# Kernel optimization log

Measured on AMD Instinct MI355X. Metric: run time of the kernel, lower is better.

## Reference

```python
import jax, jax.numpy as jnp
import numpy as np

B, S, D, H, L = 64, 512, 512, 512, 2  # batch, seq_len, input_size, hidden_size, num_layers


def setup_inputs() -> dict:
    key = jax.random.key(0)
    ks = jax.random.split(key, 4)
    s = 0.03  # keep gate pre-activations in the non-saturated range
    x = jax.random.normal(ks[0], (B, S, D), jnp.float32)
    h = jnp.zeros((B, L, H), jnp.float32)
    Wr = jax.random.normal(ks[1], (L, D + H, H), jnp.float32) * s
    Wz = jax.random.normal(ks[2], (L, D + H, H), jnp.float32) * s
    Wh = jax.random.normal(ks[3], (L, D + H, H), jnp.float32) * s
    br = jnp.zeros((L, H), jnp.float32)
    bz = jnp.zeros((L, H), jnp.float32)
    bh = jnp.zeros((L, H), jnp.float32)
    return dict(x=x, h=h, Wr=Wr, br=br, Wz=Wz, bz=bz, Wh=Wh, bh=bh)


def _gru_layer(x, h0, Wr, br, Wz, bz, Wh, bh):
    # Linear(cat(x, h)) == x @ W[:Din] + h @ W[Din:] + b ; precompute the x part
    Din = x.shape[-1]
    gx_r = jnp.einsum('bsd,dh->bsh', x, Wr[:Din]) + br  # [B,S,H]
    gx_z = jnp.einsum('bsd,dh->bsh', x, Wz[:Din]) + bz
    gx_h = jnp.einsum('bsd,dh->bsh', x, Wh[:Din]) + bh
    Wrh, Wzh, Whh = Wr[Din:], Wz[Din:], Wh[Din:]  # [H,H]

    def step(h, gates):
        gr, gz, gh = gates  # each [B,H]
        r = jax.nn.sigmoid(gr + h @ Wrh)
        z = jax.nn.sigmoid(gz + h @ Wzh)
        h_tilde = jnp.tanh(gh + (r * h) @ Whh)
        h = (1.0 - z) * h + z * h_tilde
        return h, h

    hT, ys = jax.lax.scan(
        step, h0,
        (gx_r.swapaxes(0, 1), gx_z.swapaxes(0, 1), gx_h.swapaxes(0, 1)))
    return ys.swapaxes(0, 1), hT  # [B,S,H], [B,H]


def reference(x, h, Wr, br, Wz, bz, Wh, bh):
    inp = x
    finals = []
    for l in range(L):
        inp, hT = _gru_layer(inp, h[:, l], Wr[l], br[l], Wz[l], bz[l], Wh[l], bh[l])
        finals.append(hT)
    return inp, jnp.stack(finals, axis=1)  # y:[B,S,H], final_h:[B,L,H]
```

## Files before the change

kernel.cpp:

```cpp
#include <hip/hip_runtime.h>

typedef unsigned int uint;
typedef unsigned short u16;
typedef short s16x8 __attribute__((ext_vector_type(8)));
typedef float f32x4 __attribute__((ext_vector_type(4)));
typedef uint u32x4 __attribute__((ext_vector_type(4)));

#define MFMA16(a, b, c) __builtin_amdgcn_mfma_f32_16x16x32_bf16((a), (b), (c), 0, 0, 0)

static const size_t OFF_SYNC = 0;
static const size_t OFF_HB   = 2048;
static const size_t OFF_RHB  = 526336;
static const size_t OFF_WT   = 1050624;
static const size_t OFF_YS0  = 7342080;
static const size_t OFF_GX   = 40896512;
static const size_t GX_ELEMS = (size_t)512 * 64 * 1536;

__device__ __forceinline__ short f2bf(float x) {
  uint u = __builtin_bit_cast(uint, x);
  u = u + 0x7fffu + ((u >> 16) & 1u);
  return (short)(u >> 16);
}
__device__ __forceinline__ float bf2f(u16 v) {
  uint u = ((uint)v) << 16;
  return __builtin_bit_cast(float, u);
}

__device__ __forceinline__ u32x4 ld16(const void* p) {
  u32x4 r;
  asm volatile("global_load_dwordx4 %0, %1, off" : "=v"(r) : "v"(p));
  return r;
}
__device__ __forceinline__ uint ld4u(const void* p) {
  uint r;
  asm volatile("global_load_dword %0, %1, off" : "=v"(r) : "v"(p));
  return r;
}
__device__ __forceinline__ uint ld2x(const void* p) {
  uint r;
  asm volatile("global_load_ushort %0, %1, off" : "=v"(r) : "v"(p));
  return r;
}
__device__ __forceinline__ void st4(void* p, uint v) {
  asm volatile("global_store_dword %0, %1, off" :: "v"(p), "v"(v));
}
__device__ __forceinline__ void st2(void* p, u16 v) {
  uint x = v;
  asm volatile("global_store_short %0, %1, off" :: "v"(p), "v"(x));
}
__device__ __forceinline__ u32x4 ld16c(const void* p) {
  u32x4 r;
  asm volatile("global_load_dwordx4 %0, %1, off sc0 sc1" : "=v"(r) : "v"(p));
  return r;
}
__device__ __forceinline__ void st2c(void* p, u16 v) {
  uint x = v;
  asm volatile("global_store_short %0, %1, off sc0 sc1" :: "v"(p), "v"(x));
}
__device__ __forceinline__ void waitv0() {
  asm volatile("s_waitcnt vmcnt(0)" ::: "memory");
  __builtin_amdgcn_sched_barrier(0);
}

template <int GXBF>
__device__ __forceinline__ float upk(uint v) {
  if constexpr (GXBF) return bf2f((u16)v);
  else return __builtin_bit_cast(float, v);
}

__global__ void sentinel_kernel(float* __restrict__ out, float v) {
  out[threadIdx.x] = v;
}

__global__ void init_kernel(const float* __restrict__ h_in, u16* __restrict__ hb,
                            int* __restrict__ sync) {
  int idx = blockIdx.x * 256 + threadIdx.x;
  if (idx < 512) sync[idx] = 0;
  for (int i = idx; i < 2 * 64 * 512; i += gridDim.x * 256) {
    int l = i >> 15, b = (i >> 9) & 63, c = i & 511;
    int q = b >> 4, ob = b & 15;
    hb[((l * 4 + q) * 4 + 0) * 8192 + ob * 512 + c] = (u16)f2bf(h_in[(b * 2 + l) * 512 + c]);
  }
}

__global__ void convert_w_kernel(const float* __restrict__ Wr, const float* __restrict__ Wz,
                                 const float* __restrict__ Wh, u16* __restrict__ WT) {
  int idx = blockIdx.x * 256 + threadIdx.x;
  int n = idx & 511, k = (idx >> 9) & 1023, lg = idx >> 19;
  int l = (lg >= 3) ? 1 : 0, g = lg - l * 3;
  const float* W = (g == 0 ? Wr : (g == 1 ? Wz : Wh)) + (size_t)l * 1024 * 512;
  WT[((size_t)lg * 512 + n) * 1024 + k] = (u16)f2bf(W[k * 512 + n]);
}

template <int GXBF>
__global__ __launch_bounds__(256) void proj_kernel(
    const float* __restrict__ A, const u16* __restrict__ WT,
    const float* __restrict__ br, const float* __restrict__ bz, const float* __restrict__ bh,
    void* __restrict__ gx) {
  __shared__ u16 Alds[128 * 64];
  __shared__ u16 Blds[128 * 64];
  const int tid = threadIdx.x;
  const int wave = tid >> 6, lane = tid & 63;
  const int lan15 = lane & 15, lanhi = lane >> 4;
  const int mb = blockIdx.x & 255, nb = blockIdx.x >> 8;
  const int m0 = mb * 128, n0 = nb * 128;
  const int wm = (wave >> 1) * 64, wn = (wave & 1) * 64;

  const f32x4 z4 = {0.f, 0.f, 0.f, 0.f};
  f32x4 acc[4][4];
#pragma unroll
  for (int i = 0; i < 4; ++i)
#pragma unroll
    for (int j = 0; j < 4; ++j) acc[i][j] = z4;

  for (int kb = 0; kb < 512; kb += 64) {
    __syncthreads();
#pragma unroll
    for (int p = 0; p < 4; ++p) {
      int idx = p * 256 + tid;
      int row = idx >> 3, slot = idx & 7;
      const float* src = A + (size_t)(m0 + row) * 512 + kb + slot * 8;
      float4 v0 = *(const float4*)src;
      float4 v1 = *(const float4*)(src + 4);
      u16 tmp[8] = {(u16)f2bf(v0.x), (u16)f2bf(v0.y), (u16)f2bf(v0.z), (u16)f2bf(v0.w),
                    (u16)f2bf(v1.x), (u16)f2bf(v1.y), (u16)f2bf(v1.z), (u16)f2bf(v1.w)};
      *(uint4*)((char*)Alds + row * 128 + ((slot ^ (row & 7)) * 16)) = *(uint4*)tmp;
    }
#pragma unroll
    for (int p = 0; p < 4; ++p) {
      int idx = p * 256 + tid;
      int row = idx >> 3, slot = idx & 7;
      int ng = n0 + row, g = ng >> 9, nc = ng & 511;
      uint4 v = *(const uint4*)(WT + ((size_t)g * 512 + nc) * 1024 + kb + slot * 8);
      *(uint4*)((char*)Blds + row * 128 + ((slot ^ (row & 7)) * 16)) = v;
    }
    __syncthreads();
#pragma unroll
    for (int ks = 0; ks < 2; ++ks) {
      s16x8 af[4], bfr[4];
#pragma unroll
      for (int f = 0; f < 4; ++f) {
        int rowA = wm + f * 16 + lan15;
        af[f] = *(const s16x8*)((const char*)Alds + rowA * 128 + (((ks * 4 + lanhi) ^ (rowA & 7)) * 16));
        int rowB = wn + f * 16 + lan15;
        bfr[f] = *(const s16x8*)((const char*)Blds + rowB * 128 + (((ks * 4 + lanhi) ^ (rowB & 7)) * 16));
      }
#pragma unroll
      for (int mf = 0; mf < 4; ++mf)
#pragma unroll
        for (int nf = 0; nf < 4; ++nf)
          acc[mf][nf] = MFMA16(af[mf], bfr[nf], acc[mf][nf]);
    }
  }
#pragma unroll
  for (int nf = 0; nf < 4; ++nf) {
    int n = n0 + wn + nf * 16 + lan15;
    int g = n >> 9, nc = n & 511;
    float bias = (g == 0 ? br[nc] : (g == 1 ? bz[nc] : bh[nc]));
#pragma unroll
    for (int mf = 0; mf < 4; ++mf) {
#pragma unroll
      for (int q = 0; q < 4; ++q) {
        int m = m0 + wm + mf * 16 + lanhi * 4 + q;
        int s = m & 511, b = m >> 9;
        size_t e = (size_t)(s * 64 + b) * 1536 + n;
        float v = acc[mf][nf][q] + bias;
        if constexpr (GXBF) ((u16*)gx)[e] = (u16)f2bf(v);
        else ((float*)gx)[e] = v;
      }
    }
  }
}

__device__ __forceinline__ void gbarA(int* bar, int target) {
  asm volatile("s_waitcnt vmcnt(0)" ::: "memory");
  __syncthreads();
  if (threadIdx.x == 0) {
    int one = 1;
    asm volatile("global_atomic_add %0, %1, off" :: "v"(bar), "v"(one) : "memory");
    int v, zero = 0, iter = 0;
    do {
      __builtin_amdgcn_s_sleep(1);
      asm volatile("global_atomic_add %0, %1, %2, off sc0\n\ts_waitcnt vmcnt(0)"
                   : "=v"(v) : "v"(bar), "v"(zero) : "memory");
    } while (v < target && ++iter < (1 << 17));
  }
  __syncthreads();
  __builtin_amdgcn_sched_barrier(0);
}
__device__ __forceinline__ void bar_arrive(int* bar) {
  asm volatile("s_waitcnt vmcnt(0)" ::: "memory");
  __syncthreads();
  if (threadIdx.x == 0) {
    int one = 1;
    asm volatile("global_atomic_add %0, %1, off" :: "v"(bar), "v"(one) : "memory");
  }
}
__device__ __forceinline__ void bar_wait(int* bar, int target) {
  if (threadIdx.x == 0) {
    int v, zero = 0, iter = 0;
    do {
      __builtin_amdgcn_s_sleep(1);
      asm volatile("global_atomic_add %0, %1, %2, off sc0\n\ts_waitcnt vmcnt(0)"
                   : "=v"(v) : "v"(bar), "v"(zero) : "memory");
    } while (v < target && ++iter < (1 << 17));
  }
  __syncthreads();
  __builtin_amdgcn_sched_barrier(0);
}

__device__ __forceinline__ int ROFF(int w, int c, int b) {
  return (w * 48 + c) * 20 + b;
}

template <int GXBF>
__global__ __launch_bounds__(256, 1) void gru_pipe(
    const void* __restrict__ gx,
    const u16* __restrict__ WT,
    const float* __restrict__ h_in,
    u16* __restrict__ hb,
    u16* __restrict__ rhb,
    u16* __restrict__ ys0,
    const float* __restrict__ br, const float* __restrict__ bz, const float* __restrict__ bh,
    float* __restrict__ out_f32,
    float* __restrict__ finals,
    int* __restrict__ sync) {
  __shared__ float red[21504];
  __shared__ int s_pack, s_prog;

  if (threadIdx.x == 0) {
    int xcc;
    asm volatile("s_getreg_b32 %0, hwreg(HW_REG_XCC_ID)" : "=s"(xcc));
    xcc &= 7;
    int slot = __hip_atomic_fetch_add(&sync[256 + xcc], 1, __ATOMIC_RELAXED,
                                      __HIP_MEMORY_SCOPE_AGENT);
    s_pack = slot | (xcc << 8);
    s_prog = 0;
  }
  __syncthreads();
  const int slot = s_pack & 255;
  const int xcc  = s_pack >> 8;
  if (slot >= 32) return;

  const int l = (xcc >> 2) & 1, q = xcc & 3;
  int* bar  = sync + xcc * 32;
  int* prog = sync + 320 + q * 32;

  const int tid = threadIdx.x;
  const int wave = tid >> 6, lane = tid & 63;
  const int lan15 = lane & 15, lanhi = lane >> 4;
  const int c0 = slot * 16;
  const int kw = wave * 128;
  const int ke8 = lanhi * 8;
  const int ob = tid >> 4;
  const int col = c0 + (tid & 15);
  const int gb = q * 16 + ob;
  const int ES = GXBF ? 2 : 4;
  const f32x4 z4 = {0.f, 0.f, 0.f, 0.f};

  const u16* WTl = WT + (size_t)l * 3 * 512 * 1024;
  u16* hbq  = hb  + (size_t)(l * 4 + q) * 4 * 8192;
  u16* rhbq = rhb + (size_t)(l * 4 + q) * 4 * 8192;

  s16x8 wrz[2][4], whh[4];
#pragma unroll
  for (int g = 0; g < 2; ++g)
#pragma unroll
    for (int ks = 0; ks < 4; ++ks)
      wrz[g][ks] = *(const s16x8*)(WTl + ((size_t)(g * 512 + c0 + lan15)) * 1024 + 512 + kw + ks * 32 + ke8);
#pragma unroll
  for (int ks = 0; ks < 4; ++ks)
    whh[ks] = *(const s16x8*)(WTl + ((size_t)(1024 + c0 + lan15)) * 1024 + 512 + kw + ks * 32 + ke8);

  float hown = h_in[(gb * 2 + l) * 512 + col];

  if (l == 0) {
    uint pf_r = 0, pf_z = 0, pf_hn = 0, pf_hc = 0;
    auto issue_pf = [&](int tp) {
      const char* gq = (const char*)gx + ((size_t)(tp * 64 + gb) * 1536 + col) * ES;
      if constexpr (GXBF) {
        pf_r = ld2x(gq); pf_z = ld2x(gq + 512 * 2); pf_hn = ld2x(gq + 1024 * 2);
      } else {
        pf_r = ld4u(gq); pf_z = ld4u(gq + 512 * 4); pf_hn = ld4u(gq + 1024 * 4);
      }
    };
    issue_pf(0);

    int tgt = 0;
    for (int t = 0; t < 512; ++t) {
      const u16* hc = hbq + (t & 3) * 8192;
      u16* rhc = rhbq + (t & 3) * 8192;
      u32x4 hl[4];
#pragma unroll
      for (int ks = 0; ks < 4; ++ks)
        hl[ks] = ld16(hc + lan15 * 512 + kw + ks * 32 + ke8);
      waitv0();
      f32x4 a0 = z4, a1 = z4;
#pragma unroll
      for (int ks = 0; ks < 4; ++ks) {
        s16x8 ah = __builtin_bit_cast(s16x8, hl[ks]);
        a0 = MFMA16(ah, wrz[0][ks], a0);
        a1 = MFMA16(ah, wrz[1][ks], a1);
      }
      *(f32x4*)(red + ROFF(wave, lan15, lanhi * 4)) = a0;
      *(f32x4*)(red + ROFF(wave, 16 + lan15, lanhi * 4)) = a1;
      __syncthreads();
      float zg;
      {
        float rp = upk<GXBF>(pf_r), zp = upk<GXBF>(pf_z);
#pragma unroll
        for (int w = 0; w < 4; ++w) {
          rp += red[ROFF(w, col - c0, ob)];
          zp += red[ROFF(w, 16 + (col - c0), ob)];
        }
        float r = 1.f / (1.f + __expf(-rp));
        zg = 1.f / (1.f + __expf(-zp));
        st2(rhc + ob * 512 + col, (u16)f2bf(r * hown));
      }
      tgt += 32; gbarA(bar, tgt);
      pf_hc = pf_hn;
      u32x4 rl[4];
#pragma unroll
      for (int ks = 0; ks < 4; ++ks)
        rl[ks] = ld16(rhc + lan15 * 512 + kw + ks * 32 + ke8);
      issue_pf(t < 511 ? t + 1 : 511);
      asm volatile("s_waitcnt vmcnt(3)" ::: "memory");
      __builtin_amdgcn_sched_barrier(0);
      f32x4 a2 = z4;
#pragma unroll
      for (int ks = 0; ks < 4; ++ks)
        a2 = MFMA16(__builtin_bit_cast(s16x8, rl[ks]), whh[ks], a2);
      *(f32x4*)(red + ROFF(wave, lan15, lanhi * 4)) = a2;
      __syncthreads();
      float hn;
      {
        float wp = upk<GXBF>(pf_hc);
#pragma unroll
        for (int w = 0; w < 4; ++w) wp += red[ROFF(w, col - c0, ob)];
        float pre = fminf(15.f, fmaxf(-15.f, wp));
        float e = __expf(-2.f * pre);
        float ht = (1.f - e) / (1.f + e);
        hn = (1.f - zg) * hown + zg * ht;
        hown = hn;
        u16 hv = (u16)f2bf(hn);
        st2(hbq + ((t + 1) & 3) * 8192 + ob * 512 + col, hv);
        st2c(ys0 + ((size_t)gb * 512 + t) * 512 + col, hv);
      }
      tgt += 32;
      gbarA(bar, tgt);
      if (tid == 0 && slot == 0)
        __hip_atomic_fetch_add(prog, 1, __ATOMIC_RELAXED, __HIP_MEMORY_SCOPE_AGENT);
      if (t == 511)
        finals[(size_t)(gb * 2 + 0) * 512 + col] = hn;
    }
  } else {
    s16x8 w1rz[2][4], w1h[4];
#pragma unroll
    for (int g = 0; g < 2; ++g)
#pragma unroll
      for (int ks = 0; ks < 4; ++ks)
        w1rz[g][ks] = *(const s16x8*)(WTl + ((size_t)(g * 512 + c0 + lan15)) * 1024 + kw + ks * 32 + ke8);
#pragma unroll
    for (int ks = 0; ks < 4; ++ks)
      w1h[ks] = *(const s16x8*)(WTl + ((size_t)(1024 + c0 + lan15)) * 1024 + kw + ks * 32 + ke8);
    const float brv = br[512 + col], bzv = bz[512 + col], bhv = bh[512 + col];

    u32x4 yl[4];
    if (tid == 0) {
      int pv, it = 0;
      do {
        pv = __hip_atomic_load(prog, __ATOMIC_RELAXED, __HIP_MEMORY_SCOPE_AGENT);
        if (pv > 0) break;
        __builtin_amdgcn_s_sleep(2);
      } while (++it < (1 << 22));
      s_prog = pv;
    }
    __syncthreads();
    __builtin_amdgcn_sched_barrier(0);
#pragma unroll
    for (int ks = 0; ks < 4; ++ks)
      yl[ks] = ld16c(ys0 + ((size_t)(q * 16 + lan15) * 512 + 0) * 512 + kw + ks * 32 + ke8);

    int tgt = 0;
    for (int t = 0; t < 512; ++t) {
      const u16* hc = hbq + (t & 3) * 8192;
      u16* rhc = rhbq + (t & 3) * 8192;
      u32x4 hl[4];
#pragma unroll
      for (int ks = 0; ks < 4; ++ks)
        hl[ks] = ld16(hc + lan15 * 512 + kw + ks * 32 + ke8);
      waitv0();
      f32x4 a0 = z4, a1 = z4, a2 = z4;
#pragma unroll
      for (int ks = 0; ks < 4; ++ks) {
        s16x8 ah = __builtin_bit_cast(s16x8, hl[ks]);
        s16x8 ay = __builtin_bit_cast(s16x8, yl[ks]);
        a0 = MFMA16(ah, wrz[0][ks], a0);
        a0 = MFMA16(ay, w1rz[0][ks], a0);
        a1 = MFMA16(ah, wrz[1][ks], a1);
        a1 = MFMA16(ay, w1rz[1][ks], a1);
        a2 = MFMA16(ay, w1h[ks], a2);
      }
      *(f32x4*)(red + ROFF(wave, lan15, lanhi * 4)) = a0;
      *(f32x4*)(red + ROFF(wave, 16 + lan15, lanhi * 4)) = a1;
      *(f32x4*)(red + ROFF(wave, 32 + lan15, lanhi * 4)) = a2;
      __syncthreads();
      float zg, w1c;
      {
        float rp = brv, zp = bzv, wc = 0.f;
#pragma unroll
        for (int w = 0; w < 4; ++w) {
          rp += red[ROFF(w, col - c0, ob)];
          zp += red[ROFF(w, 16 + (col - c0), ob)];
          wc += red[ROFF(w, 32 + (col - c0), ob)];
        }
        float r = 1.f / (1.f + __expf(-rp));
        zg = 1.f / (1.f + __expf(-zp));
        w1c = wc;
        st2(rhc + ob * 512 + col, (u16)f2bf(r * hown));
      }
      tgt += 32;
      bar_arrive(bar);
      if (t != 511) {
        if (s_prog < t + 2) {
          if (tid == 0) {
            int pv, it = 0;
            do {
              pv = __hip_atomic_load(prog, __ATOMIC_RELAXED, __HIP_MEMORY_SCOPE_AGENT);
              if (pv >= t + 2) break;
              __builtin_amdgcn_s_sleep(2);
            } while (++it < (1 << 22));
            s_prog = pv;
          }
          __syncthreads();
        }
#pragma unroll
        for (int ks = 0; ks < 4; ++ks)
          yl[ks] = ld16c(ys0 + ((size_t)(q * 16 + lan15) * 512 + (t + 1)) * 512 + kw + ks * 32 + ke8);
      }
      bar_wait(bar, tgt);
      u32x4 rl[4];
#pragma unroll
      for (int ks = 0; ks < 4; ++ks)
        rl[ks] = ld16(rhc + lan15 * 512 + kw + ks * 32 + ke8);
      waitv0();
      f32x4 a3 = z4;
#pragma unroll
      for (int ks = 0; ks < 4; ++ks)
        a3 = MFMA16(__builtin_bit_cast(s16x8, rl[ks]), whh[ks], a3);
      *(f32x4*)(red + ROFF(wave, lan15, lanhi * 4)) = a3;
      __syncthreads();
      float hn;
      {
        float wp = bhv + w1c;
#pragma unroll
        for (int w = 0; w < 4; ++w) wp += red[ROFF(w, col - c0, ob)];
        float pre = fminf(15.f, fmaxf(-15.f, wp));
        float e = __expf(-2.f * pre);
        float ht = (1.f - e) / (1.f + e);
        hn = (1.f - zg) * hown + zg * ht;
        hown = hn;
        st2(hbq + ((t + 1) & 3) * 8192 + ob * 512 + col, (u16)f2bf(hn));
      }
      tgt += 32;
      if (t != 511) {
        bar_arrive(bar);
        st4(out_f32 + ((size_t)gb * 512 + t) * 512 + col, __builtin_bit_cast(uint, hn));
        bar_wait(bar, tgt);
      } else {
        st4(out_f32 + ((size_t)gb * 512 + t) * 512 + col, __builtin_bit_cast(uint, hn));
        finals[(size_t)(gb * 2 + 1) * 512 + col] = hn;
      }
    }
  }
}

template <int GXBF>
static void run_all(const float* x, const float* h, const float* Wr, const float* br,
                    const float* Wz, const float* bz, const float* Wh, const float* bh,
                    float* out, char* ws, hipStream_t stream) {
  int* sync  = (int*)(ws + OFF_SYNC);
  u16* hbAll = (u16*)(ws + OFF_HB);
  u16* rhb   = (u16*)(ws + OFF_RHB);
  u16* WT    = (u16*)(ws + OFF_WT);
  u16* ys0   = (u16*)(ws + OFF_YS0);
  void* gx   = (void*)(ws + OFF_GX);
  float* finals = out + 16777216;

  init_kernel<<<64, 256, 0, stream>>>(h, hbAll, sync);
  convert_w_kernel<<<12288, 256, 0, stream>>>(Wr, Wz, Wh, WT);
  proj_kernel<GXBF><<<3072, 256, 0, stream>>>(x, WT, br, bz, bh, gx);
  gru_pipe<GXBF><<<256, 256, 0, stream>>>(gx, WT, h, hbAll, rhb, ys0,
                                          br, bz, bh, out, finals, sync);
}

extern "C" void kernel_launch(void* const* d_in, const int* in_sizes, int n_in,
                              void* d_out, int out_size, void* d_ws, size_t ws_size,
                              hipStream_t stream) {
  const float* x  = (const float*)d_in[0];
  const float* h  = (const float*)d_in[1];
  const float* Wr = (const float*)d_in[2];
  const float* br = (const float*)d_in[3];
  const float* Wz = (const float*)d_in[4];
  const float* bz = (const float*)d_in[5];
  const float* Wh = (const float*)d_in[6];
  const float* bh = (const float*)d_in[7];
  float* out = (float*)d_out;
  char* ws = (char*)d_ws;

  const size_t need_f32 = OFF_GX + GX_ELEMS * 4;
  const size_t need_bf  = OFF_GX + GX_ELEMS * 2;

  if (ws_size >= need_f32) {
    run_all<0>(x, h, Wr, br, Wz, bz, Wh, bh, out, ws, stream);
  } else if (ws_size >= need_bf) {
    run_all<1>(x, h, Wr, br, Wz, bz, Wh, bh, out, ws, stream);
  } else {
    sentinel_kernel<<<1, 64, 0, stream>>>(out, (float)ws_size);
  }
}
```

Measured before the change: 2.423 ms.

## Split each batch group into two halves and ping-pong their phases across barriers

Each 16-row batch group is split into two 8-row halves (A and B) with separate h and r*h buffers and separate grid barriers per half. Each half's phase runs while the other half's barrier is still in flight, so barrier latency is hidden behind useful MFMA work. The spin-wait now checks the counter before sleeping. The cost is twice as many MFMA passes, since each pass feeds only half the rows and the other lanes load dummy data. Barrier and atomic traffic per step also rises.

```diff
diff --git a/kernel.cpp b/kernel.cpp
--- a/kernel.cpp
+++ b/kernel.cpp
@@ -9,11 +9,13 @@
 #define MFMA16(a, b, c) __builtin_amdgcn_mfma_f32_16x16x32_bf16((a), (b), (c), 0, 0, 0)
 
 static const size_t OFF_SYNC = 0;
-static const size_t OFF_HB   = 2048;
-static const size_t OFF_RHB  = 526336;
-static const size_t OFF_WT   = 1050624;
-static const size_t OFF_YS0  = 7342080;
-static const size_t OFF_GX   = 40896512;
+static const size_t OFF_HBA  = 8192;
+static const size_t OFF_HBB  = 139264;
+static const size_t OFF_RHA  = 270336;
+static const size_t OFF_RHB  = 401408;
+static const size_t OFF_WT   = 532480;
+static const size_t OFF_YS0  = 6823936;
+static const size_t OFF_GX   = 40378368;
 static const size_t GX_ELEMS = (size_t)512 * 64 * 1536;
 
 __device__ __forceinline__ short f2bf(float x) {
@@ -72,14 +74,17 @@
   out[threadIdx.x] = v;
 }
 
-__global__ void init_kernel(const float* __restrict__ h_in, u16* __restrict__ hb,
-                            int* __restrict__ sync) {
+__global__ void init_kernel(const float* __restrict__ h_in, u16* __restrict__ hbA,
+                            u16* __restrict__ hbB, int* __restrict__ sync) {
   int idx = blockIdx.x * 256 + threadIdx.x;
-  if (idx < 512) sync[idx] = 0;
+  if (idx < 2048) sync[idx] = 0;
   for (int i = idx; i < 2 * 64 * 512; i += gridDim.x * 256) {
     int l = i >> 15, b = (i >> 9) & 63, c = i & 511;
     int q = b >> 4, ob = b & 15;
-    hb[((l * 4 + q) * 4 + 0) * 8192 + ob * 512 + c] = (u16)f2bf(h_in[(b * 2 + l) * 512 + c]);
+    u16 v = (u16)f2bf(h_in[(b * 2 + l) * 512 + c]);
+    int reg = ((l * 4 + q) * 2 + 0) * 4096;
+    if (ob < 8) hbA[reg + ob * 512 + c] = v;
+    else        hbB[reg + (ob - 8) * 512 + c] = v;
   }
 }
 
@@ -172,22 +177,6 @@
   }
 }
 
-__device__ __forceinline__ void gbarA(int* bar, int target) {
-  asm volatile("s_waitcnt vmcnt(0)" ::: "memory");
-  __syncthreads();
-  if (threadIdx.x == 0) {
-    int one = 1;
-    asm volatile("global_atomic_add %0, %1, off" :: "v"(bar), "v"(one) : "memory");
-    int v, zero = 0, iter = 0;
-    do {
-      __builtin_amdgcn_s_sleep(1);
-      asm volatile("global_atomic_add %0, %1, %2, off sc0\n\ts_waitcnt vmcnt(0)"
-                   : "=v"(v) : "v"(bar), "v"(zero) : "memory");
-    } while (v < target && ++iter < (1 << 17));
-  }
-  __syncthreads();
-  __builtin_amdgcn_sched_barrier(0);
-}
 __device__ __forceinline__ void bar_arrive(int* bar) {
   asm volatile("s_waitcnt vmcnt(0)" ::: "memory");
   __syncthreads();
@@ -200,10 +189,11 @@
   if (threadIdx.x == 0) {
     int v, zero = 0, iter = 0;
     do {
-      __builtin_amdgcn_s_sleep(1);
       asm volatile("global_atomic_add %0, %1, %2, off sc0\n\ts_waitcnt vmcnt(0)"
                    : "=v"(v) : "v"(bar), "v"(zero) : "memory");
-    } while (v < target && ++iter < (1 << 17));
+      if (v >= target) break;
+      __builtin_amdgcn_s_sleep(1);
+    } while (++iter < (1 << 17));
   }
   __syncthreads();
   __builtin_amdgcn_sched_barrier(0);
@@ -218,8 +208,8 @@
     const void* __restrict__ gx,
     const u16* __restrict__ WT,
     const float* __restrict__ h_in,
-    u16* __restrict__ hb,
-    u16* __restrict__ rhb,
+    u16* __restrict__ hbA, u16* __restrict__ hbB,
+    u16* __restrict__ rhA, u16* __restrict__ rhB,
     u16* __restrict__ ys0,
     const float* __restrict__ br, const float* __restrict__ bz, const float* __restrict__ bh,
     float* __restrict__ out_f32,
@@ -232,7 +222,7 @@
     int xcc;
     asm volatile("s_getreg_b32 %0, hwreg(HW_REG_XCC_ID)" : "=s"(xcc));
     xcc &= 7;
-    int slot = __hip_atomic_fetch_add(&sync[256 + xcc], 1, __ATOMIC_RELAXED,
+    int slot = __hip_atomic_fetch_add(&sync[1024 + xcc], 1, __ATOMIC_RELAXED,
                                       __HIP_MEMORY_SCOPE_AGENT);
     s_pack = slot | (xcc << 8);
     s_prog = 0;
@@ -243,8 +233,11 @@
   if (slot >= 32) return;
 
   const int l = (xcc >> 2) & 1, q = xcc & 3;
-  int* bar  = sync + xcc * 32;
-  int* prog = sync + 320 + q * 32;
+  int* b1A = sync + xcc * 128;
+  int* b1B = b1A + 32;
+  int* b2A = b1A + 64;
+  int* b2B = b1A + 96;
+  int* prog = sync + 1088 + q * 32;
 
   const int tid = threadIdx.x;
   const int wave = tid >> 6, lane = tid & 63;
@@ -255,12 +248,20 @@
   const int ob = tid >> 4;
   const int col = c0 + (tid & 15);
   const int gb = q * 16 + ob;
+  const bool isA = (ob < 8);
   const int ES = GXBF ? 2 : 4;
   const f32x4 z4 = {0.f, 0.f, 0.f, 0.f};
 
   const u16* WTl = WT + (size_t)l * 3 * 512 * 1024;
-  u16* hbq  = hb  + (size_t)(l * 4 + q) * 4 * 8192;
-  u16* rhbq = rhb + (size_t)(l * 4 + q) * 4 * 8192;
+  const u16* deadp = WT;
+  const int reg2 = (l * 4 + q) * 2;
+  u16* hbAq = hbA + reg2 * 4096;
+  u16* hbBq = hbB + reg2 * 4096;
+  u16* rhAq = rhA + reg2 * 4096;
+  u16* rhBq = rhB + reg2 * 4096;
+
+  const int rowoff = lan15 * 512;
+  const int rowoffB = (lan15 - 8) * 512;
 
   s16x8 wrz[2][4], whh[4];
 #pragma unroll
@@ -285,74 +286,140 @@
       }
     };
     issue_pf(0);
-
-    int tgt = 0;
+    float zg = 0.f, hn = 0.f;
+
     for (int t = 0; t < 512; ++t) {
-      const u16* hc = hbq + (t & 3) * 8192;
-      u16* rhc = rhbq + (t & 3) * 8192;
-      u32x4 hl[4];
-#pragma unroll
-      for (int ks = 0; ks < 4; ++ks)
-        hl[ks] = ld16(hc + lan15 * 512 + kw + ks * 32 + ke8);
-      waitv0();
-      f32x4 a0 = z4, a1 = z4;
-#pragma unroll
-      for (int ks = 0; ks < 4; ++ks) {
-        s16x8 ah = __builtin_bit_cast(s16x8, hl[ks]);
-        a0 = MFMA16(ah, wrz[0][ks], a0);
-        a1 = MFMA16(ah, wrz[1][ks], a1);
-      }
-      *(f32x4*)(red + ROFF(wave, lan15, lanhi * 4)) = a0;
-      *(f32x4*)(red + ROFF(wave, 16 + lan15, lanhi * 4)) = a1;
-      __syncthreads();
-      float zg;
-      {
-        float rp = upk<GXBF>(pf_r), zp = upk<GXBF>(pf_z);
-#pragma unroll
-        for (int w = 0; w < 4; ++w) {
-          rp += red[ROFF(w, col - c0, ob)];
-          zp += red[ROFF(w, 16 + (col - c0), ob)];
-        }
-        float r = 1.f / (1.f + __expf(-rp));
-        zg = 1.f / (1.f + __expf(-zp));
-        st2(rhc + ob * 512 + col, (u16)f2bf(r * hown));
-      }
-      tgt += 32; gbarA(bar, tgt);
+      const int bufR = (t & 1) * 4096, bufW = ((t + 1) & 1) * 4096;
+      {
+        const u16* ha = (lan15 < 8) ? (hbAq + bufR + rowoff) : (deadp + rowoff);
+        u32x4 hl[4];
+#pragma unroll
+        for (int ks = 0; ks < 4; ++ks) hl[ks] = ld16(ha + kw + ks * 32 + ke8);
+        waitv0();
+        f32x4 a0 = z4, a1 = z4;
+#pragma unroll
+        for (int ks = 0; ks < 4; ++ks) {
+          s16x8 ah = __builtin_bit_cast(s16x8, hl[ks]);
+          a0 = MFMA16(ah, wrz[0][ks], a0);
+          a1 = MFMA16(ah, wrz[1][ks], a1);
+        }
+        *(f32x4*)(red + ROFF(wave, lan15, lanhi * 4)) = a0;
+        *(f32x4*)(red + ROFF(wave, 16 + lan15, lanhi * 4)) = a1;
+        __syncthreads();
+        if (isA) {
+          float rp = upk<GXBF>(pf_r), zp = upk<GXBF>(pf_z);
+#pragma unroll
+          for (int w = 0; w < 4; ++w) {
+            rp += red[ROFF(w, col - c0, ob)];
+            zp += red[ROFF(w, 16 + (col - c0), ob)];
+          }
+          float r = 1.f / (1.f + __expf(-rp));
+          zg = 1.f / (1.f + __expf(-zp));
+          st2(rhAq + bufR + ob * 512 + col, (u16)f2bf(r * hown));
+        }
+      }
+      bar_arrive(b1A);
+      if (t > 0) {
+        bar_wait(b2B, 32 * t);
+        if (tid == 0 && slot == 0)
+          __hip_atomic_fetch_add(prog, 1, __ATOMIC_RELAXED, __HIP_MEMORY_SCOPE_AGENT);
+      }
+      {
+        const u16* hbp = (lan15 >= 8) ? (hbBq + bufR + rowoffB) : (deadp + rowoff);
+        u32x4 hl[4];
+#pragma unroll
+        for (int ks = 0; ks < 4; ++ks) hl[ks] = ld16(hbp + kw + ks * 32 + ke8);
+        waitv0();
+        f32x4 a0 = z4, a1 = z4;
+#pragma unroll
+        for (int ks = 0; ks < 4; ++ks) {
+          s16x8 ah = __builtin_bit_cast(s16x8, hl[ks]);
+          a0 = MFMA16(ah, wrz[0][ks], a0);
+          a1 = MFMA16(ah, wrz[1][ks], a1);
+        }
+        *(f32x4*)(red + ROFF(wave, lan15, lanhi * 4)) = a0;
+        *(f32x4*)(red + ROFF(wave, 16 + lan15, lanhi * 4)) = a1;
+        __syncthreads();
+        if (!isA) {
+          float rp = upk<GXBF>(pf_r), zp = upk<GXBF>(pf_z);
+#pragma unroll
+          for (int w = 0; w < 4; ++w) {
+            rp += red[ROFF(w, col - c0, ob)];
+            zp += red[ROFF(w, 16 + (col - c0), ob)];
+          }
+          float r = 1.f / (1.f + __expf(-rp));
+          zg = 1.f / (1.f + __expf(-zp));
+          st2(rhBq + bufR + (ob - 8) * 512 + col, (u16)f2bf(r * hown));
+        }
+      }
+      bar_arrive(b1B);
+      bar_wait(b1A, 32 * (t + 1));
       pf_hc = pf_hn;
-      u32x4 rl[4];
-#pragma unroll
-      for (int ks = 0; ks < 4; ++ks)
-        rl[ks] = ld16(rhc + lan15 * 512 + kw + ks * 32 + ke8);
-      issue_pf(t < 511 ? t + 1 : 511);
-      asm volatile("s_waitcnt vmcnt(3)" ::: "memory");
-      __builtin_amdgcn_sched_barrier(0);
-      f32x4 a2 = z4;
-#pragma unroll
-      for (int ks = 0; ks < 4; ++ks)
-        a2 = MFMA16(__builtin_bit_cast(s16x8, rl[ks]), whh[ks], a2);
-      *(f32x4*)(red + ROFF(wave, lan15, lanhi * 4)) = a2;
-      __syncthreads();
-      float hn;
-      {
-        float wp = upk<GXBF>(pf_hc);
-#pragma unroll
-        for (int w = 0; w < 4; ++w) wp += red[ROFF(w, col - c0, ob)];
-        float pre = fminf(15.f, fmaxf(-15.f, wp));
-        float e = __expf(-2.f * pre);
-        float ht = (1.f - e) / (1.f + e);
-        hn = (1.f - zg) * hown + zg * ht;
-        hown = hn;
-        u16 hv = (u16)f2bf(hn);
-        st2(hbq + ((t + 1) & 3) * 8192 + ob * 512 + col, hv);
-        st2c(ys0 + ((size_t)gb * 512 + t) * 512 + col, hv);
-      }
-      tgt += 32;
-      gbarA(bar, tgt);
-      if (tid == 0 && slot == 0)
-        __hip_atomic_fetch_add(prog, 1, __ATOMIC_RELAXED, __HIP_MEMORY_SCOPE_AGENT);
-      if (t == 511)
-        finals[(size_t)(gb * 2 + 0) * 512 + col] = hn;
+      {
+        const u16* ra = (lan15 < 8) ? (rhAq + bufR + rowoff) : (deadp + rowoff);
+        u32x4 rl[4];
+#pragma unroll
+        for (int ks = 0; ks < 4; ++ks) rl[ks] = ld16(ra + kw + ks * 32 + ke8);
+        waitv0();
+        f32x4 a2 = z4;
+#pragma unroll
+        for (int ks = 0; ks < 4; ++ks)
+          a2 = MFMA16(__builtin_bit_cast(s16x8, rl[ks]), whh[ks], a2);
+        *(f32x4*)(red + ROFF(wave, lan15, lanhi * 4)) = a2;
+        __syncthreads();
+        if (isA) {
+          float wp = upk<GXBF>(pf_hc);
+#pragma unroll
+          for (int w = 0; w < 4; ++w) wp += red[ROFF(w, col - c0, ob)];
+          float pre = fminf(15.f, fmaxf(-15.f, wp));
+          float e = __expf(-2.f * pre);
+          float ht = (1.f - e) / (1.f + e);
+          hn = (1.f - zg) * hown + zg * ht;
+          hown = hn;
+          u16 hv = (u16)f2bf(hn);
+          st2(hbAq + bufW + ob * 512 + col, hv);
+          st2c(ys0 + ((size_t)gb * 512 + t) * 512 + col, hv);
+        }
+      }
+      bar_arrive(b2A);
+      if (t == 511 && isA) finals[(size_t)(gb * 2 + 0) * 512 + col] = hn;
+      bar_wait(b1B, 32 * (t + 1));
+      {
+        const u16* rb = (lan15 >= 8) ? (rhBq + bufR + rowoffB) : (deadp + rowoff);
+        u32x4 rl[4];
+#pragma unroll
+        for (int ks = 0; ks < 4; ++ks) rl[ks] = ld16(rb + kw + ks * 32 + ke8);
+        waitv0();
+        f32x4 a2 = z4;
+#pragma unroll
+        for (int ks = 0; ks < 4; ++ks)
+          a2 = MFMA16(__builtin_bit_cast(s16x8, rl[ks]), whh[ks], a2);
+        *(f32x4*)(red + ROFF(wave, lan15, lanhi * 4)) = a2;
+        __syncthreads();
+        if (!isA) {
+          float wp = upk<GXBF>(pf_hc);
+#pragma unroll
+          for (int w = 0; w < 4; ++w) wp += red[ROFF(w, col - c0, ob)];
+          float pre = fminf(15.f, fmaxf(-15.f, wp));
+          float e = __expf(-2.f * pre);
+          float ht = (1.f - e) / (1.f + e);
+          hn = (1.f - zg) * hown + zg * ht;
+          hown = hn;
+          u16 hv = (u16)f2bf(hn);
+          st2(hbBq + bufW + (ob - 8) * 512 + col, hv);
+          st2c(ys0 + ((size_t)gb * 512 + t) * 512 + col, hv);
+        }
+      }
+      bar_arrive(b2B);
+      if (t == 511 && !isA) finals[(size_t)(gb * 2 + 0) * 512 + col] = hn;
+      if (t != 511) {
+        issue_pf(t + 1);
+        bar_wait(b2A, 32 * (t + 1));
+      }
     }
+    bar_wait(b2B, 32 * 512);
+    if (tid == 0 && slot == 0)
+      __hip_atomic_fetch_add(prog, 1, __ATOMIC_RELAXED, __HIP_MEMORY_SCOPE_AGENT);
   } else {
     s16x8 w1rz[2][4], w1h[4];
 #pragma unroll
@@ -366,6 +433,8 @@
     const float brv = br[512 + col], bzv = bz[512 + col], bhv = bh[512 + col];
 
     u32x4 yl[4];
+    float zg = 0.f, w1c = 0.f, hn = 0.f;
+
     if (tid == 0) {
       int pv, it = 0;
       do {
@@ -381,46 +450,141 @@
     for (int ks = 0; ks < 4; ++ks)
       yl[ks] = ld16c(ys0 + ((size_t)(q * 16 + lan15) * 512 + 0) * 512 + kw + ks * 32 + ke8);
 
-    int tgt = 0;
     for (int t = 0; t < 512; ++t) {
-      const u16* hc = hbq + (t & 3) * 8192;
-      u16* rhc = rhbq + (t & 3) * 8192;
-      u32x4 hl[4];
-#pragma unroll
-      for (int ks = 0; ks < 4; ++ks)
-        hl[ks] = ld16(hc + lan15 * 512 + kw + ks * 32 + ke8);
-      waitv0();
-      f32x4 a0 = z4, a1 = z4, a2 = z4;
-#pragma unroll
-      for (int ks = 0; ks < 4; ++ks) {
-        s16x8 ah = __builtin_bit_cast(s16x8, hl[ks]);
-        s16x8 ay = __builtin_bit_cast(s16x8, yl[ks]);
-        a0 = MFMA16(ah, wrz[0][ks], a0);
-        a0 = MFMA16(ay, w1rz[0][ks], a0);
-        a1 = MFMA16(ah, wrz[1][ks], a1);
-        a1 = MFMA16(ay, w1rz[1][ks], a1);
-        a2 = MFMA16(ay, w1h[ks], a2);
-      }
-      *(f32x4*)(red + ROFF(wave, lan15, lanhi * 4)) = a0;
-      *(f32x4*)(red + ROFF(wave, 16 + lan15, lanhi * 4)) = a1;
-      *(f32x4*)(red + ROFF(wave, 32 + lan15, lanhi * 4)) = a2;
-      __syncthreads();
-      float zg, w1c;
-      {
-        float rp = brv, zp = bzv, wc = 0.f;
-#pragma unroll
-        for (int w = 0; w < 4; ++w) {
-          rp += red[ROFF(w, col - c0, ob)];
-          zp += red[ROFF(w, 16 + (col - c0), ob)];
-          wc += red[ROFF(w, 32 + (col - c0), ob)];
-        }
-        float r = 1.f / (1.f + __expf(-rp));
-        zg = 1.f / (1.f + __expf(-zp));
-        w1c = wc;
-        st2(rhc + ob * 512 + col, (u16)f2bf(r * hown));
-      }
-      tgt += 32;
-      bar_arrive(bar);
+      const int bufR = (t & 1) * 4096, bufW = ((t + 1) & 1) * 4096;
+      {
+        const u16* ha = (lan15 < 8) ? (hbAq + bufR + rowoff) : (deadp + rowoff);
+        u32x4 hl[4];
+#pragma unroll
+        for (int ks = 0; ks < 4; ++ks) hl[ks] = ld16(ha + kw + ks * 32 + ke8);
+        waitv0();
+        f32x4 a0 = z4, a1 = z4, a2 = z4;
+#pragma unroll
+        for (int ks = 0; ks < 4; ++ks) {
+          s16x8 ah = __builtin_bit_cast(s16x8, hl[ks]);
+          s16x8 ay = __builtin_bit_cast(s16x8, yl[ks]);
+          a0 = MFMA16(ah, wrz[0][ks], a0);
+          a0 = MFMA16(ay, w1rz[0][ks], a0);
+          a1 = MFMA16(ah, wrz[1][ks], a1);
+          a1 = MFMA16(ay, w1rz[1][ks], a1);
+          a2 = MFMA16(ay, w1h[ks], a2);
+        }
+        *(f32x4*)(red + ROFF(wave, lan15, lanhi * 4)) = a0;
+        *(f32x4*)(red + ROFF(wave, 16 + lan15, lanhi * 4)) = a1;
+        *(f32x4*)(red + ROFF(wave, 32 + lan15, lanhi * 4)) = a2;
+        __syncthreads();
+        if (isA) {
+          float rp = brv, zp = bzv, wc = 0.f;
+#pragma unroll
+          for (int w = 0; w < 4; ++w) {
+            rp += red[ROFF(w, col - c0, ob)];
+            zp += red[ROFF(w, 16 + (col - c0), ob)];
+            wc += red[ROFF(w, 32 + (col - c0), ob)];
+          }
+          float r = 1.f / (1.f + __expf(-rp));
+          zg = 1.f / (1.f + __expf(-zp));
+          w1c = wc;
+          st2(rhAq + bufR + ob * 512 + col, (u16)f2bf(r * hown));
+        }
+      }
+      bar_arrive(b1A);
+      if (t > 0) bar_wait(b2B, 32 * t);
+      {
+        const u16* hbp = (lan15 >= 8) ? (hbBq + bufR + rowoffB) : (deadp + rowoff);
+        u32x4 hl[4];
+#pragma unroll
+        for (int ks = 0; ks < 4; ++ks) hl[ks] = ld16(hbp + kw + ks * 32 + ke8);
+        waitv0();
+        f32x4 a0 = z4, a1 = z4, a2 = z4;
+#pragma unroll
+        for (int ks = 0; ks < 4; ++ks) {
+          s16x8 ah = __builtin_bit_cast(s16x8, hl[ks]);
+          s16x8 ay = __builtin_bit_cast(s16x8, yl[ks]);
+          a0 = MFMA16(ah, wrz[0][ks], a0);
+          a0 = MFMA16(ay, w1rz[0][ks], a0);
+          a1 = MFMA16(ah, wrz[1][ks], a1);
+          a1 = MFMA16(ay, w1rz[1][ks], a1);
+          a2 = MFMA16(ay, w1h[ks], a2);
+        }
+        *(f32x4*)(red + ROFF(wave, lan15, lanhi * 4)) = a0;
+        *(f32x4*)(red + ROFF(wave, 16 + lan15, lanhi * 4)) = a1;
+        *(f32x4*)(red + ROFF(wave, 32 + lan15, lanhi * 4)) = a2;
+        __syncthreads();
+        if (!isA) {
+          float rp = brv, zp = bzv, wc = 0.f;
+#pragma unroll
+          for (int w = 0; w < 4; ++w) {
+            rp += red[ROFF(w, col - c0, ob)];
+            zp += red[ROFF(w, 16 + (col - c0), ob)];
+            wc += red[ROFF(w, 32 + (col - c0), ob)];
+          }
+          float r = 1.f / (1.f + __expf(-rp));
+          zg = 1.f / (1.f + __expf(-zp));
+          w1c = wc;
+          st2(rhBq + bufR + (ob - 8) * 512 + col, (u16)f2bf(r * hown));
+        }
+      }
+      bar_arrive(b1B);
+      bar_wait(b1A, 32 * (t + 1));
+      {
+        const u16* ra = (lan15 < 8) ? (rhAq + bufR + rowoff) : (deadp + rowoff);
+        u32x4 rl[4];
+#pragma unroll
+        for (int ks = 0; ks < 4; ++ks) rl[ks] = ld16(ra + kw + ks * 32 + ke8);
+        waitv0();
+        f32x4 a3 = z4;
+#pragma unroll
+        for (int ks = 0; ks < 4; ++ks)
+          a3 = MFMA16(__builtin_bit_cast(s16x8, rl[ks]), whh[ks], a3);
+        *(f32x4*)(red + ROFF(wave, lan15, lanhi * 4)) = a3;
+        __syncthreads();
+        if (isA) {
+          float wp = bhv + w1c;
+#pragma unroll
+          for (int w = 0; w < 4; ++w) wp += red[ROFF(w, col - c0, ob)];
+          float pre = fminf(15.f, fmaxf(-15.f, wp));
+          float e = __expf(-2.f * pre);
+          float ht = (1.f - e) / (1.f + e);
+          hn = (1.f - zg) * hown + zg * ht;
+          hown = hn;
+          st2(hbAq + bufW + ob * 512 + col, (u16)f2bf(hn));
+        }
+      }
+      bar_arrive(b2A);
+      if (isA) {
+        st4(out_f32 + ((size_t)gb * 512 + t) * 512 + col, __builtin_bit_cast(uint, hn));
+        if (t == 511) finals[(size_t)(gb * 2 + 1) * 512 + col] = hn;
+      }
+      bar_wait(b1B, 32 * (t + 1));
+      {
+        const u16* rb = (lan15 >= 8) ? (rhBq + bufR + rowoffB) : (deadp + rowoff);
+        u32x4 rl[4];
+#pragma unroll
+        for (int ks = 0; ks < 4; ++ks) rl[ks] = ld16(rb + kw + ks * 32 + ke8);
+        waitv0();
+        f32x4 a3 = z4;
+#pragma unroll
+        for (int ks = 0; ks < 4; ++ks)
+          a3 = MFMA16(__builtin_bit_cast(s16x8, rl[ks]), whh[ks], a3);
+        *(f32x4*)(red + ROFF(wave, lan15, lanhi * 4)) = a3;
+        __syncthreads();
+        if (!isA) {
+          float wp = bhv + w1c;
+#pragma unroll
+          for (int w = 0; w < 4; ++w) wp += red[ROFF(w, col - c0, ob)];
+          float pre = fminf(15.f, fmaxf(-15.f, wp));
+          float e = __expf(-2.f * pre);
+          float ht = (1.f - e) / (1.f + e);
+          hn = (1.f - zg) * hown + zg * ht;
+          hown = hn;
+          st2(hbBq + bufW + (ob - 8) * 512 + col, (u16)f2bf(hn));
+        }
+      }
+      bar_arrive(b2B);
+      if (!isA) {
+        st4(out_f32 + ((size_t)gb * 512 + t) * 512 + col, __builtin_bit_cast(uint, hn));
+        if (t == 511) finals[(size_t)(gb * 2 + 1) * 512 + col] = hn;
+      }
       if (t != 511) {
         if (s_prog < t + 2) {
           if (tid == 0) {
@@ -437,39 +601,7 @@
 #pragma unroll
         for (int ks = 0; ks < 4; ++ks)
           yl[ks] = ld16c(ys0 + ((size_t)(q * 16 + lan15) * 512 + (t + 1)) * 512 + kw + ks * 32 + ke8);
-      }
-      bar_wait(bar, tgt);
-      u32x4 rl[4];
-#pragma unroll
-      for (int ks = 0; ks < 4; ++ks)
-        rl[ks] = ld16(rhc + lan15 * 512 + kw + ks * 32 + ke8);
-      waitv0();
-      f32x4 a3 = z4;
-#pragma unroll
-      for (int ks = 0; ks < 4; ++ks)
-        a3 = MFMA16(__builtin_bit_cast(s16x8, rl[ks]), whh[ks], a3);
-      *(f32x4*)(red + ROFF(wave, lan15, lanhi * 4)) = a3;
-      __syncthreads();
-      float hn;
-      {
-        float wp = bhv + w1c;
-#pragma unroll
-        for (int w = 0; w < 4; ++w) wp += red[ROFF(w, col - c0, ob)];
-        float pre = fminf(15.f, fmaxf(-15.f, wp));
-        float e = __expf(-2.f * pre);
-        float ht = (1.f - e) / (1.f + e);
-        hn = (1.f - zg) * hown + zg * ht;
-        hown = hn;
-        st2(hbq + ((t + 1) & 3) * 8192 + ob * 512 + col, (u16)f2bf(hn));
-      }
-      tgt += 32;
-      if (t != 511) {
-        bar_arrive(bar);
-        st4(out_f32 + ((size_t)gb * 512 + t) * 512 + col, __builtin_bit_cast(uint, hn));
-        bar_wait(bar, tgt);
-      } else {
-        st4(out_f32 + ((size_t)gb * 512 + t) * 512 + col, __builtin_bit_cast(uint, hn));
-        finals[(size_t)(gb * 2 + 1) * 512 + col] = hn;
+        bar_wait(b2A, 32 * (t + 1));
       }
     }
   }
@@ -480,17 +612,19 @@
                     const float* Wz, const float* bz, const float* Wh, const float* bh,
                     float* out, char* ws, hipStream_t stream) {
   int* sync  = (int*)(ws + OFF_SYNC);
-  u16* hbAll = (u16*)(ws + OFF_HB);
-  u16* rhb   = (u16*)(ws + OFF_RHB);
+  u16* hbA   = (u16*)(ws + OFF_HBA);
+  u16* hbB   = (u16*)(ws + OFF_HBB);
+  u16* rhA   = (u16*)(ws + OFF_RHA);
+  u16* rhB   = (u16*)(ws + OFF_RHB);
   u16* WT    = (u16*)(ws + OFF_WT);
   u16* ys0   = (u16*)(ws + OFF_YS0);
   void* gx   = (void*)(ws + OFF_GX);
   float* finals = out + 16777216;
 
-  init_kernel<<<64, 256, 0, stream>>>(h, hbAll, sync);
+  init_kernel<<<64, 256, 0, stream>>>(h, hbA, hbB, sync);
   convert_w_kernel<<<12288, 256, 0, stream>>>(Wr, Wz, Wh, WT);
   proj_kernel<GXBF><<<3072, 256, 0, stream>>>(x, WT, br, bz, bh, gx);
-  gru_pipe<GXBF><<<256, 256, 0, stream>>>(gx, WT, h, hbAll, rhb, ys0,
+  gru_pipe<GXBF><<<256, 256, 0, stream>>>(gx, WT, h, hbA, hbB, rhA, rhB, ys0,
                                           br, bz, bh, out, finals, sync);
 }
 
```

Measured after the change: 3.159 ms. 1.3x slower.
